# Performance work log

Hardware: AMD Instinct MI355X
Metric: run time of the kernel (lower is better)

The kernel has to match this reference:

```python
import jax, jax.numpy as jnp
import numpy as np

N, E = 50000, 800000
IN, HID, HEADS, LAT = 128, 64, 4, 32
NEG_SLOPE = 0.2  # PyG GATv2Conv default negative_slope


def _glorot(key, shape):
    fan_in, fan_out = shape[0], shape[-1]
    lim = (6.0 / (fan_in + fan_out)) ** 0.5
    return jax.random.uniform(key, shape, jnp.float32, -lim, lim)


def setup_inputs() -> dict:
    keys = jax.random.split(jax.random.key(0), 10)
    x = jax.random.normal(keys[0], (N, IN), jnp.float32)
    edge_index = jax.random.randint(keys[1], (2, E), 0, N, jnp.int32)
    return {
        "x": x,
        "edge_index": edge_index,
        # layer 1: in -> hidden, heads=HEADS, concat=True
        "W_l1": _glorot(keys[2], (IN, HEADS * HID)),
        "W_r1": _glorot(keys[3], (IN, HEADS * HID)),
        "att1": _glorot(keys[4], (HEADS, HID)),
        "bias1": jnp.zeros((HEADS * HID,), jnp.float32),
        # layer 2: heads*hidden -> latent, heads=1, concat=False
        "W_l2": _glorot(keys[5], (HEADS * HID, LAT)),
        "W_r2": _glorot(keys[6], (HEADS * HID, LAT)),
        "att2": _glorot(keys[7], (1, LAT)),
        "bias2": jnp.zeros((LAT,), jnp.float32),
    }


def gatv2_layer(x, src, dst, W_l, W_r, att, bias, heads, out_ch, concat):
    """PyG GATv2Conv (eval mode, add_self_loops already applied to src/dst)."""
    n = x.shape[0]
    xl = (x @ W_l).reshape(n, heads, out_ch)  # source transform (messages)
    xr = (x @ W_r).reshape(n, heads, out_ch)  # target transform
    # per-edge attention logits: a^T LeakyReLU(xl[j] + xr[i])
    e = jax.nn.leaky_relu(xl[src] + xr[dst], NEG_SLOPE)  # [E, H, C]
    score = jnp.einsum('ehc,hc->eh', e, att)             # [E, H]
    # segment softmax over incoming edges of each dst node
    smax = jax.ops.segment_max(score, dst, num_segments=n)   # [N, H]
    ex = jnp.exp(score - smax[dst])
    denom = jax.ops.segment_sum(ex, dst, num_segments=n)     # [N, H]
    alpha = ex / denom[dst]                                  # [E, H]
    # scatter-add weighted source features
    out = jax.ops.segment_sum(xl[src] * alpha[..., None], dst, num_segments=n)
    out = out.reshape(n, heads * out_ch) if concat else out.mean(axis=1)
    return out + bias


def reference(x, edge_index, W_l1, W_r1, att1, bias1, W_l2, W_r2, att2, bias2):
    n = x.shape[0]
    # GATv2Conv adds self loops by default
    loops = jnp.arange(n, dtype=edge_index.dtype)
    src = jnp.concatenate([edge_index[0], loops])
    dst = jnp.concatenate([edge_index[1], loops])
    h = jax.nn.elu(gatv2_layer(x, src, dst, W_l1, W_r1, att1, bias1, HEADS, HID, True))
    z = gatv2_layer(h, src, dst, W_l2, W_r2, att2, bias2, 1, LAT, False)
    # decode: sigmoid(<z[row], z[col]>) over the original edges
    row, col = edge_index[0], edge_index[1]
    pred = jax.nn.sigmoid(jnp.sum(z[row] * z[col], axis=1))
    return pred
```

## Files before the change

### kernel.cpp

```cpp
#include <hip/hip_runtime.h>
#include <hip/hip_fp16.h>
#include <math.h>

#define N_NODES 50000
#define N_EDGES 800000
#define EP (N_EDGES + N_NODES)
#define IN_CH 128
#define HID 64
#define HEADS 4
#define F1 (HEADS * HID)
#define LAT 32
#define NEG 0.2f
#define CAP 64

typedef __attribute__((ext_vector_type(8))) short short8;
typedef __attribute__((ext_vector_type(8))) unsigned short ushort8v;
typedef __attribute__((ext_vector_type(4))) float f32x4;

__device__ __forceinline__ unsigned short f2bf(float f) {
    unsigned int x = __float_as_uint(f);
    x += 0x7fffu + ((x >> 16) & 1u);
    return (unsigned short)(x >> 16);
}
__device__ __forceinline__ float bf2f(unsigned short u) {
    return __uint_as_float(((unsigned int)u) << 16);
}
__device__ __forceinline__ float h2f(unsigned short u) {
    return __half2float(__ushort_as_half(u));
}
__device__ __forceinline__ f32x4 mfma_bf16(short8 a, short8 b, f32x4 c) {
    return __builtin_amdgcn_mfma_f32_16x16x32_bf16(a, b, c, 0, 0, 0);
}

__global__ void conv_w(const float* __restrict__ Wl1, const float* __restrict__ Wr1,
                       const float* __restrict__ Wl2, const float* __restrict__ Wr2,
                       unsigned short* __restrict__ Wt1, unsigned short* __restrict__ Wt2) {
    int idx = blockIdx.x * 256 + threadIdx.x;
    if (idx < 512 * 128) {
        int n = idx >> 7, k = idx & 127;
        float v = (n < 256) ? Wl1[(size_t)k * 256 + n] : Wr1[(size_t)k * 256 + (n - 256)];
        Wt1[idx] = f2bf(v);
    } else if (idx < 512 * 128 + 64 * 256) {
        int j = idx - 512 * 128;
        int n = j >> 8, k = j & 255;
        float v = (n < 32) ? Wl2[(size_t)k * 32 + n] : Wr2[(size_t)k * 32 + (n - 32)];
        Wt2[j] = f2bf(v);
    }
}

__global__ __launch_bounds__(256) void gemm1_mfma(const float* __restrict__ x,
                                                  const unsigned short* __restrict__ Wt1,
                                                  unsigned short* __restrict__ xlh,
                                                  unsigned short* __restrict__ xrh) {
    int wave = threadIdx.x >> 6;
    int lane = threadIdx.x & 63;
    int quad = lane >> 4, lo = lane & 15;
    int row0 = blockIdx.x * 32;
    int colw = wave * 128;
    int rB0 = min(row0 + lo, N_NODES - 1);
    int rB1 = min(row0 + 16 + lo, N_NODES - 1);
    f32x4 acc[2][8];
#pragma unroll
    for (int rt = 0; rt < 2; rt++)
#pragma unroll
        for (int ct = 0; ct < 8; ct++) acc[rt][ct] = (f32x4){0.f, 0.f, 0.f, 0.f};
#pragma unroll
    for (int ks = 0; ks < 4; ks++) {
        int koff = ks * 32 + quad * 8;
        float4 fa0 = *(const float4*)(x + (size_t)rB0 * IN_CH + koff);
        float4 fb0 = *(const float4*)(x + (size_t)rB0 * IN_CH + koff + 4);
        float4 fa1 = *(const float4*)(x + (size_t)rB1 * IN_CH + koff);
        float4 fb1 = *(const float4*)(x + (size_t)rB1 * IN_CH + koff + 4);
        short8 b0, b1;
        b0[0] = f2bf(fa0.x); b0[1] = f2bf(fa0.y); b0[2] = f2bf(fa0.z); b0[3] = f2bf(fa0.w);
        b0[4] = f2bf(fb0.x); b0[5] = f2bf(fb0.y); b0[6] = f2bf(fb0.z); b0[7] = f2bf(fb0.w);
        b1[0] = f2bf(fa1.x); b1[1] = f2bf(fa1.y); b1[2] = f2bf(fa1.z); b1[3] = f2bf(fa1.w);
        b1[4] = f2bf(fb1.x); b1[5] = f2bf(fb1.y); b1[6] = f2bf(fb1.z); b1[7] = f2bf(fb1.w);
#pragma unroll
        for (int ct = 0; ct < 8; ct++) {
            short8 a = *(const short8*)(Wt1 + (size_t)(colw + ct * 16 + lo) * IN_CH + koff);
            acc[0][ct] = mfma_bf16(a, b0, acc[0][ct]);
            acc[1][ct] = mfma_bf16(a, b1, acc[1][ct]);
        }
    }
#pragma unroll
    for (int rt = 0; rt < 2; rt++) {
        int node = row0 + rt * 16 + lo;
        if (node < N_NODES) {
#pragma unroll
            for (int ct = 0; ct < 8; ct++) {
                int feat = colw + ct * 16 + quad * 4;
                ushort4 u;
                u.x = f2bf(acc[rt][ct][0]); u.y = f2bf(acc[rt][ct][1]);
                u.z = f2bf(acc[rt][ct][2]); u.w = f2bf(acc[rt][ct][3]);
                if (feat < F1)
                    *(ushort4*)(xlh + (size_t)node * F1 + feat) = u;
                else
                    *(ushort4*)(xrh + (size_t)node * F1 + (feat - F1)) = u;
            }
        }
    }
}

__global__ void scatter_bucket(const int* __restrict__ ei, int* __restrict__ cnt,
                               int* __restrict__ srcsP) {
    long e = (long)blockIdx.x * 256 + threadIdx.x;
    if (e >= EP) return;
    int s, d;
    if (e < N_EDGES) { s = ei[e]; d = ei[N_EDGES + e]; }
    else             { s = d = (int)(e - N_EDGES); }
    int pos = atomicAdd(&cnt[d], 1);
    if (pos < CAP) srcsP[(d << 6) + pos] = s;
}

__global__ __launch_bounds__(256) void fused_l1(const unsigned short* __restrict__ xlh,
                                                const unsigned short* __restrict__ xrh,
                                                unsigned short* __restrict__ hbf,
                                                const int* __restrict__ srcsP,
                                                const int* __restrict__ cnt,
                                                const float* __restrict__ att,
                                                const float* __restrict__ bias) {
    int wave = threadIdx.x >> 6;
    int lane = threadIdx.x & 63;
    int h = lane >> 5;
    int c = lane & 31;
    int c0 = c << 3;
    int d = blockIdx.x * 4 + wave;
    if (d >= N_NODES) return;
    ushort8v xru = *(const ushort8v*)(xrh + (size_t)d * F1 + c0);
    float4 atA = *(const float4*)(att + c0);
    float4 atB = *(const float4*)(att + c0 + 4);
    float xr8[8], at8[8] = {atA.x, atA.y, atA.z, atA.w, atB.x, atB.y, atB.z, atB.w};
#pragma unroll
    for (int i = 0; i < 8; i++) xr8[i] = bf2f(xru[i]);
    int start = d << 6;
    int dg    = min(CAP, __builtin_amdgcn_readfirstlane(cnt[d]));
    float l = 0.f;
    float acc[8] = {};
    int jj = h;
    int s = srcsP[start + jj];
    ushort8v raw = *(const ushort8v*)(xlh + (size_t)s * F1 + c0);
    int sN = srcsP[start + jj + 2];
    int iters = (dg + 1) >> 1;
    for (int k = 0; k < iters; k++) {
        ushort8v cr = raw;
        raw = *(const ushort8v*)(xlh + (size_t)sN * F1 + c0);
        sN = srcsP[start + jj + 4];
        float a[8];
#pragma unroll
        for (int i = 0; i < 8; i++) a[i] = bf2f(cr[i]);
        float sc = 0.f;
#pragma unroll
        for (int i = 0; i < 8; i++) {
            float v = a[i] + xr8[i];
            v = fmaxf(v, NEG * v);
            sc += v * at8[i];
        }
        sc += __shfl_xor(sc, 1);
        sc += __shfl_xor(sc, 2);
        sc += __shfl_xor(sc, 4);
        float ex = (jj < dg) ? __expf(sc) : 0.f;
        l += ex;
#pragma unroll
        for (int i = 0; i < 8; i++) acc[i] += ex * a[i];
        jj += 2;
    }
    l += __shfl_xor(l, 32);
#pragma unroll
    for (int i = 0; i < 8; i++) acc[i] += __shfl_xor(acc[i], 32);
    if (h == 0) {
        float inv = 1.0f / l;
        float4 bA = *(const float4*)(bias + c0);
        float4 bB = *(const float4*)(bias + c0 + 4);
        float b8[8] = {bA.x, bA.y, bA.z, bA.w, bB.x, bB.y, bB.z, bB.w};
        ushort8v ho;
#pragma unroll
        for (int i = 0; i < 8; i++) {
            float o = acc[i] * inv + b8[i];
            o = o > 0.f ? o : __expf(o) - 1.0f;
            ho[i] = (unsigned short)f2bf(o);
        }
        *(ushort8v*)(hbf + (size_t)d * F1 + c0) = ho;
    }
}

__global__ __launch_bounds__(256) void gemm2_mfma(const unsigned short* __restrict__ hbf,
                                                  const unsigned short* __restrict__ Wt2,
                                                  __half* __restrict__ xl2h,
                                                  float* __restrict__ xr2) {
    int wave = threadIdx.x >> 6;
    int lane = threadIdx.x & 63;
    int quad = lane >> 4, lo = lane & 15;
    int row0 = blockIdx.x * 64 + wave * 16;
    int rB = min(row0 + lo, N_NODES - 1);
    f32x4 acc[4];
#pragma unroll
    for (int ct = 0; ct < 4; ct++) acc[ct] = (f32x4){0.f, 0.f, 0.f, 0.f};
#pragma unroll
    for (int ks = 0; ks < 8; ks++) {
        int koff = ks * 32 + quad * 8;
        short8 b = *(const short8*)(hbf + (size_t)rB * F1 + koff);
#pragma unroll
        for (int ct = 0; ct < 4; ct++) {
            short8 a = *(const short8*)(Wt2 + (size_t)(ct * 16 + lo) * F1 + koff);
            acc[ct] = mfma_bf16(a, b, acc[ct]);
        }
    }
    int node = row0 + lo;
    if (node < N_NODES) {
#pragma unroll
        for (int ct = 0; ct < 4; ct++) {
            int feat = ct * 16 + quad * 4;
            if (feat < LAT) {
                ushort4 u;
                u.x = __half_as_ushort(__float2half_rn(acc[ct][0]));
                u.y = __half_as_ushort(__float2half_rn(acc[ct][1]));
                u.z = __half_as_ushort(__float2half_rn(acc[ct][2]));
                u.w = __half_as_ushort(__float2half_rn(acc[ct][3]));
                *(ushort4*)((unsigned short*)xl2h + (size_t)node * LAT + feat) = u;
            } else {
                float4 f = make_float4(acc[ct][0], acc[ct][1], acc[ct][2], acc[ct][3]);
                *(float4*)(xr2 + (size_t)node * LAT + (feat - LAT)) = f;
            }
        }
    }
}

__global__ __launch_bounds__(256) void fused_l2(const __half* __restrict__ xl2h,
                                                const float* __restrict__ xr2,
                                                const int* __restrict__ srcsP,
                                                const int* __restrict__ cnt,
                                                const float* __restrict__ att,
                                                const float* __restrict__ bias,
                                                __half* __restrict__ zh) {
    int wave = threadIdx.x >> 6;
    int lane = threadIdx.x & 63;
    int q = lane >> 4;
    int c = lane & 15;
    int c2 = c << 1;
    int d = blockIdx.x * 4 + wave;
    if (d >= N_NODES) return;
    float xr0 = xr2[(size_t)d * LAT + c2];
    float xr1v = xr2[(size_t)d * LAT + c2 + 1];
    float av0 = att[c2], av1 = att[c2 + 1];
    int start = d << 6;
    int dg    = min(CAP, __builtin_amdgcn_readfirstlane(cnt[d]));
    float l = 0.f, acc0 = 0.f, acc1 = 0.f;
    int jj = q;
    int s = srcsP[start + jj];
    __half2 raw = *(const __half2*)(xl2h + (size_t)s * LAT + c2);
    int sN = srcsP[start + jj + 4];
    int iters = (dg + 3) >> 2;
    for (int k = 0; k < iters; k++) {
        __half2 cr = raw;
        raw = *(const __half2*)(xl2h + (size_t)sN * LAT + c2);
        sN = srcsP[start + jj + 8];
        float a0 = __half2float(cr.x), a1 = __half2float(cr.y);
        float v0 = a0 + xr0;  v0 = fmaxf(v0, NEG * v0);
        float v1 = a1 + xr1v; v1 = fmaxf(v1, NEG * v1);
        float sc = v0 * av0 + v1 * av1;
        sc += __shfl_xor(sc, 1);
        sc += __shfl_xor(sc, 2);
        sc += __shfl_xor(sc, 4);
        sc += __shfl_xor(sc, 8);
        float ex = (jj < dg) ? __expf(sc) : 0.f;
        l += ex;
        acc0 += ex * a0;
        acc1 += ex * a1;
        jj += 4;
    }
    l += __shfl_xor(l, 16); acc0 += __shfl_xor(acc0, 16); acc1 += __shfl_xor(acc1, 16);
    l += __shfl_xor(l, 32); acc0 += __shfl_xor(acc0, 32); acc1 += __shfl_xor(acc1, 32);
    if (q == 0) {
        __half2 o;
        o.x = __float2half_rn(acc0 / l + bias[c2]);
        o.y = __float2half_rn(acc1 / l + bias[c2 + 1]);
        *(__half2*)(zh + (size_t)d * LAT + c2) = o;
    }
}

__global__ __launch_bounds__(256) void decode(const __half* __restrict__ zh,
                                              const int* __restrict__ ei,
                                              float* __restrict__ out) {
    int g = threadIdx.x >> 2;
    int lane = threadIdx.x & 3;
    long e = (long)blockIdx.x * 64 + g;
    if (e >= N_EDGES) return;
    int r = ei[e], c = ei[N_EDGES + e];
    int cc = lane << 3;
    ushort8v ur = *(const ushort8v*)((const unsigned short*)zh + (size_t)r * LAT + cc);
    ushort8v uc = *(const ushort8v*)((const unsigned short*)zh + (size_t)c * LAT + cc);
    float v = 0.f;
#pragma unroll
    for (int i = 0; i < 8; i++) {
        v += h2f(ur[i]) * h2f(uc[i]);
    }
    v += __shfl_xor(v, 1);
    v += __shfl_xor(v, 2);
    if (lane == 0) out[e] = 1.0f / (1.0f + __expf(-v));
}

extern "C" void kernel_launch(void* const* d_in, const int* in_sizes, int n_in,
                              void* d_out, int out_size, void* d_ws, size_t ws_size,
                              hipStream_t stream) {
    const float* x    = (const float*)d_in[0];
    const int*   ei   = (const int*)d_in[1];
    const float* Wl1  = (const float*)d_in[2];
    const float* Wr1  = (const float*)d_in[3];
    const float* att1 = (const float*)d_in[4];
    const float* b1   = (const float*)d_in[5];
    const float* Wl2  = (const float*)d_in[6];
    const float* Wr2  = (const float*)d_in[7];
    const float* att2 = (const float*)d_in[8];
    const float* b2   = (const float*)d_in[9];
    float* out = (float*)d_out;

    unsigned short* xrh = (unsigned short*)d_ws;
    unsigned short* hbf = xrh + (size_t)N_NODES * F1;
    unsigned short* xlh = hbf + (size_t)N_NODES * F1;
    int* cnt   = (int*)(xlh + (size_t)N_NODES * F1);
    int* srcsP = cnt + N_NODES;
    unsigned short* Wt1 = (unsigned short*)(srcsP + (size_t)N_NODES * CAP + 16);
    unsigned short* Wt2 = Wt1 + 512 * 128;
    __half* xl2h = (__half*)xlh;
    float*  xr2  = (float*)(xl2h + (size_t)N_NODES * LAT);
    __half* zh   = (__half*)(xr2 + (size_t)N_NODES * LAT);

    conv_w<<<(512 * 128 + 64 * 256 + 255) / 256, 256, 0, stream>>>(Wl1, Wr1, Wl2, Wr2,
                                                                   Wt1, Wt2);
    hipMemsetAsync(cnt, 0, ((size_t)N_NODES * (CAP + 1) + 16) * sizeof(int), stream);

    gemm1_mfma<<<(N_NODES + 31) / 32, 256, 0, stream>>>(x, Wt1, xlh, xrh);

    scatter_bucket<<<(EP + 255) / 256, 256, 0, stream>>>(ei, cnt, srcsP);

    fused_l1<<<(N_NODES + 3) / 4, 256, 0, stream>>>(xlh, xrh, hbf, srcsP, cnt, att1, b1);

    gemm2_mfma<<<(N_NODES + 63) / 64, 256, 0, stream>>>(hbf, Wt2, xl2h, xr2);
    fused_l2<<<(N_NODES + 3) / 4, 256, 0, stream>>>(xl2h, xr2, srcsP, cnt, att2, b2, zh);

    decode<<<(N_EDGES + 63) / 64, 256, 0, stream>>>(zh, ei, out);
}
```

Before: 325.4 us.

## Fuse memset into weight convert, merge scatter into GEMM1, store 16-bit sources

The separate memset is folded into the weight-conversion kernel, which now also zeroes the degree counters and neighbour buckets with int4 stores. The scatter-bucket work is appended as extra blocks of the first GEMM launch, so the two independent jobs share one launch and can overlap. Neighbour source indices are stored as unsigned 16-bit values, since the node count fits in that range. This halves bucket memory traffic in the zeroing, scatter and both aggregation kernels. The cost is hard-coded sizes, and the code now assumes fewer than 65536 nodes.

```diff
diff --git a/kernel.cpp b/kernel.cpp
--- a/kernel.cpp
+++ b/kernel.cpp
@@ -12,6 +12,10 @@
 #define LAT 32
 #define NEG 0.2f
 #define CAP 64
+#define NW (512 * 128 + 64 * 256)
+#define G1B ((N_NODES + 31) / 32)
+#define SCB ((EP + 255) / 256)
+#define ZQ 412502
 
 typedef __attribute__((ext_vector_type(8))) short short8;
 typedef __attribute__((ext_vector_type(8))) unsigned short ushort8v;
@@ -32,15 +36,17 @@
     return __builtin_amdgcn_mfma_f32_16x16x32_bf16(a, b, c, 0, 0, 0);
 }
 
-__global__ void conv_w(const float* __restrict__ Wl1, const float* __restrict__ Wr1,
-                       const float* __restrict__ Wl2, const float* __restrict__ Wr2,
-                       unsigned short* __restrict__ Wt1, unsigned short* __restrict__ Wt2) {
+__global__ void conv_w_zero(const float* __restrict__ Wl1, const float* __restrict__ Wr1,
+                            const float* __restrict__ Wl2, const float* __restrict__ Wr2,
+                            unsigned short* __restrict__ Wt1, unsigned short* __restrict__ Wt2,
+                            int4* __restrict__ zbase) {
     int idx = blockIdx.x * 256 + threadIdx.x;
+    if (idx < ZQ) zbase[idx] = make_int4(0, 0, 0, 0);
     if (idx < 512 * 128) {
         int n = idx >> 7, k = idx & 127;
         float v = (n < 256) ? Wl1[(size_t)k * 256 + n] : Wr1[(size_t)k * 256 + (n - 256)];
         Wt1[idx] = f2bf(v);
-    } else if (idx < 512 * 128 + 64 * 256) {
+    } else if (idx < NW) {
         int j = idx - 512 * 128;
         int n = j >> 8, k = j & 255;
         float v = (n < 32) ? Wl2[(size_t)k * 32 + n] : Wr2[(size_t)k * 32 + (n - 32)];
@@ -48,10 +54,23 @@
     }
 }
 
-__global__ __launch_bounds__(256) void gemm1_mfma(const float* __restrict__ x,
-                                                  const unsigned short* __restrict__ Wt1,
-                                                  unsigned short* __restrict__ xlh,
-                                                  unsigned short* __restrict__ xrh) {
+__global__ __launch_bounds__(256) void gemm1_scatter(
+    const float* __restrict__ x, const unsigned short* __restrict__ Wt1,
+    unsigned short* __restrict__ xlh, unsigned short* __restrict__ xrh,
+    const int* __restrict__ ei, int* __restrict__ cnt,
+    unsigned short* __restrict__ srcsP)
+{
+    if (blockIdx.x >= G1B) {
+        long e = (long)(blockIdx.x - G1B) * 256 + threadIdx.x;
+        if (e < EP) {
+            int s, d;
+            if (e < N_EDGES) { s = ei[e]; d = ei[N_EDGES + e]; }
+            else             { s = d = (int)(e - N_EDGES); }
+            int pos = atomicAdd(&cnt[d], 1);
+            if (pos < CAP) srcsP[(d << 6) + pos] = (unsigned short)s;
+        }
+        return;
+    }
     int wave = threadIdx.x >> 6;
     int lane = threadIdx.x & 63;
     int quad = lane >> 4, lo = lane & 15;
@@ -102,21 +121,10 @@
     }
 }
 
-__global__ void scatter_bucket(const int* __restrict__ ei, int* __restrict__ cnt,
-                               int* __restrict__ srcsP) {
-    long e = (long)blockIdx.x * 256 + threadIdx.x;
-    if (e >= EP) return;
-    int s, d;
-    if (e < N_EDGES) { s = ei[e]; d = ei[N_EDGES + e]; }
-    else             { s = d = (int)(e - N_EDGES); }
-    int pos = atomicAdd(&cnt[d], 1);
-    if (pos < CAP) srcsP[(d << 6) + pos] = s;
-}
-
 __global__ __launch_bounds__(256) void fused_l1(const unsigned short* __restrict__ xlh,
                                                 const unsigned short* __restrict__ xrh,
                                                 unsigned short* __restrict__ hbf,
-                                                const int* __restrict__ srcsP,
+                                                const unsigned short* __restrict__ srcsP,
                                                 const int* __restrict__ cnt,
                                                 const float* __restrict__ att,
                                                 const float* __restrict__ bias) {
@@ -228,7 +236,7 @@
 
 __global__ __launch_bounds__(256) void fused_l2(const __half* __restrict__ xl2h,
                                                 const float* __restrict__ xr2,
-                                                const int* __restrict__ srcsP,
+                                                const unsigned short* __restrict__ srcsP,
                                                 const int* __restrict__ cnt,
                                                 const float* __restrict__ att,
                                                 const float* __restrict__ bias,
@@ -318,21 +326,18 @@
     unsigned short* xrh = (unsigned short*)d_ws;
     unsigned short* hbf = xrh + (size_t)N_NODES * F1;
     unsigned short* xlh = hbf + (size_t)N_NODES * F1;
-    int* cnt   = (int*)(xlh + (size_t)N_NODES * F1);
-    int* srcsP = cnt + N_NODES;
-    unsigned short* Wt1 = (unsigned short*)(srcsP + (size_t)N_NODES * CAP + 16);
+    int* cnt = (int*)(xlh + (size_t)N_NODES * F1);
+    unsigned short* srcsP = (unsigned short*)(cnt + N_NODES);
+    unsigned short* Wt1 = srcsP + (size_t)N_NODES * CAP + 16;
     unsigned short* Wt2 = Wt1 + 512 * 128;
     __half* xl2h = (__half*)xlh;
     float*  xr2  = (float*)(xl2h + (size_t)N_NODES * LAT);
     __half* zh   = (__half*)(xr2 + (size_t)N_NODES * LAT);
 
-    conv_w<<<(512 * 128 + 64 * 256 + 255) / 256, 256, 0, stream>>>(Wl1, Wr1, Wl2, Wr2,
-                                                                   Wt1, Wt2);
-    hipMemsetAsync(cnt, 0, ((size_t)N_NODES * (CAP + 1) + 16) * sizeof(int), stream);
-
-    gemm1_mfma<<<(N_NODES + 31) / 32, 256, 0, stream>>>(x, Wt1, xlh, xrh);
-
-    scatter_bucket<<<(EP + 255) / 256, 256, 0, stream>>>(ei, cnt, srcsP);
+    conv_w_zero<<<(ZQ + 255) / 256, 256, 0, stream>>>(Wl1, Wr1, Wl2, Wr2, Wt1, Wt2,
+                                                      (int4*)cnt);
+
+    gemm1_scatter<<<G1B + SCB, 256, 0, stream>>>(x, Wt1, xlh, xrh, ei, cnt, srcsP);
 
     fused_l1<<<(N_NODES + 3) / 4, 256, 0, stream>>>(xlh, xrh, hbf, srcsP, cnt, att1, b1);
 
```

After: 323.9 us. No clear change (-0.5%).
